# Performance work log

Hardware: AMD Instinct MI355X
Metric: run time of the kernel (lower is better)

The kernel has to match this reference:

```python
import jax, jax.numpy as jnp
import numpy as np

B, N, D = 16, 2048, 128  # batch, nodes, embedding_dim

def setup_inputs() -> dict:
    key = jax.random.key(0)
    ks = jax.random.split(key, 12)
    def dense(kw, kb, din, dout):
        # keras Dense default glorot_uniform weight, zeros bias (use small random bias for generality)
        lim = np.sqrt(6.0 / (din + dout))
        W = jax.random.uniform(kw, (din, dout), minval=-lim, maxval=lim, dtype=jnp.float32)
        b = jax.random.normal(kb, (dout,), dtype=jnp.float32) * 0.01
        return W, b
    Wq, bq = dense(ks[0], ks[1], D, D)
    Wk, bk = dense(ks[2], ks[3], D, D)
    Wv, bv = dense(ks[4], ks[5], D, D)
    Wo, bo = dense(ks[6], ks[7], D, D)
    query_ = jax.random.normal(ks[8], (B, N, D), dtype=jnp.float32)
    key_ = jax.random.normal(ks[9], (B, N, D), dtype=jnp.float32)
    mask = jax.random.randint(ks[10], (B, N + 1, N + 1), 0, 2).astype(bool)
    return {"query_": query_, "key_": key_, "mask": mask,
            "Wq": Wq, "bq": bq, "Wk": Wk, "bk": bk,
            "Wv": Wv, "bv": bv, "Wo": Wo, "bo": bo}

def reference(query_, key_, mask, Wq, bq, Wk, bk, Wv, bv, Wo, bo):
    q = query_ @ Wq + bq                       # [B,N,D]
    k = key_ @ Wk + bk                         # [B,N,D]
    comp = jnp.einsum('bqd,bkd->bqk', q, k)    # [B,N,N]
    comp = comp / jnp.sqrt(jnp.asarray(k.shape[-1], jnp.float32))
    m = mask[:, 1:, 1:]                        # [B,N,N]
    comp = jnp.where(m, -jnp.inf, comp)
    attn = jax.nn.softmax(comp, axis=-1)
    attn = jnp.where(jnp.isnan(attn), 0.0, attn)  # fully-masked rows -> 0
    # NOTE: faithful to source: value projection applied to the PROJECTED key
    v = k @ Wv + bv                            # [B,N,D]
    out = jnp.einsum('bqk,bkd->bqd', attn, v)
    return out @ Wo + bo
```

## Files before the change

### kernel.cpp

```cpp
#include <hip/hip_runtime.h>

#define SB 16
#define SN 2048
#define SD 128
#define NM 2049
#define SZ (SB*SN*SD)
#define WLDS 17408

typedef __bf16 bf16x8 __attribute__((ext_vector_type(8)));
typedef float f32x4 __attribute__((ext_vector_type(4)));

__device__ __forceinline__ unsigned short f2b(float f){
  union { float f; unsigned int u; } v; v.f = f;
  unsigned int r = v.u + 0x7fffu + ((v.u >> 16) & 1u);
  return (unsigned short)(r >> 16);
}
__device__ __forceinline__ unsigned short f2b_fast(float f){
  union { float f; unsigned int u; } v; v.f = f;
  return (unsigned short)((v.u + 0x8000u) >> 16);
}

__device__ __forceinline__ void async16(const void* g, void* l){
  __builtin_amdgcn_global_load_lds(
      (__attribute__((address_space(1))) void*)(g),
      (__attribute__((address_space(3))) void*)(l), 16, 0, 0);
}

__global__ __launch_bounds__(256) void prep_pack_kernel(
    const float* __restrict__ Wq, const float* __restrict__ Wk,
    const float* __restrict__ Wv, const float* __restrict__ Wo,
    const int* __restrict__ mask,
    unsigned short* __restrict__ wts, unsigned long long* __restrict__ pm)
{
  if (blockIdx.x < 64){
    int widx = blockIdx.x >> 4;
    int kg   = blockIdx.x & 15;
    const float* W = (widx==0)?Wq:(widx==1)?Wk:(widx==2)?Wv:Wo;
    unsigned short* O = wts + widx*16384;
    int t = threadIdx.x;
    int k = kg*8 + (t>>5);
    int n = (t&31)*4;
    float4 v = *reinterpret_cast<const float4*>(W + k*SD + n);
    O[(n+0)*SD + k] = f2b(v.x);
    O[(n+1)*SD + k] = f2b(v.y);
    O[(n+2)*SD + k] = f2b(v.z);
    O[(n+3)*SD + k] = f2b(v.w);
    return;
  }
  int widx = blockIdx.x - 64;
  int wave = widx*4 + (threadIdx.x>>6);
  int ln = threadIdx.x & 63;
  size_t wb0 = (size_t)wave*256;
  for (int rr=0; rr<32; rr++){
    size_t wb = wb0 + rr*8;
    int v[8];
    for (int i=0;i<8;i++){
      size_t wbi = wb + i;
      int bb = (int)(wbi>>16); int rem = (int)(wbi & 65535);
      int row = rem>>5; int kt = rem&31;
      v[i] = mask[(size_t)bb*NM*NM + (size_t)(row+1)*NM + 1 + kt*64 + ln];
    }
    unsigned long long bt[8];
    for (int i=0;i<8;i++) bt[i] = __ballot(v[i]!=0);
    if (ln==0){
      for (int i=0;i<4;i++){
        ulonglong2 t; t.x = bt[2*i]; t.y = bt[2*i+1];
        *reinterpret_cast<ulonglong2*>(&pm[wb + 2*i]) = t;
      }
    }
  }
}

__global__ __launch_bounds__(256) void qkv_kernel(
    const float* __restrict__ query, const float* __restrict__ key,
    const unsigned short* __restrict__ wts,
    const float* __restrict__ bq, const float* __restrict__ bk,
    const float* __restrict__ bv,
    unsigned short* __restrict__ qb, unsigned short* __restrict__ kb,
    unsigned short* __restrict__ vt)
{
  __shared__ unsigned short lds[2*WLDS + 9216];
  int tid=threadIdx.x;
  int w=tid>>6, ln=tid&63, g=ln>>4, lm=ln&15;
  bool isq = blockIdx.x < 512;
  int id = isq ? blockIdx.x : (blockIdx.x - 512);
  int bb = id>>5, n0 = (id&31)*64;
  size_t rowbase = (size_t)bb*SN + n0 + w*16;
  const float sc = 0.08838834764831845f;

  if (isq){
    for (int i=0;i<8;i++){
      int p = i*256+tid; int row=p>>4, c=p&15;
      uint4 t = *reinterpret_cast<const uint4*>(wts + p*8);
      *reinterpret_cast<uint4*>(&lds[row*136 + c*8]) = t;
    }
    __syncthreads();
    float bqv[8];
    for (int d=0;d<8;d++) bqv[d] = bq[d*16+lm];
    const float* xr = query + (rowbase + lm)*SD;
    bf16x8 af[4];
    for (int ks=0;ks<4;ks++){
      float4 x0 = *reinterpret_cast<const float4*>(xr + ks*32 + g*8);
      float4 x1 = *reinterpret_cast<const float4*>(xr + ks*32 + g*8 + 4);
      union { bf16x8 v; unsigned short s[8]; } u;
      u.s[0]=f2b(x0.x); u.s[1]=f2b(x0.y); u.s[2]=f2b(x0.z); u.s[3]=f2b(x0.w);
      u.s[4]=f2b(x1.x); u.s[5]=f2b(x1.y); u.s[6]=f2b(x1.z); u.s[7]=f2b(x1.w);
      af[ks]=u.v;
    }
    for (int d=0; d<8; d++){
      f32x4 acc = {0.f,0.f,0.f,0.f};
      for (int ks=0;ks<4;ks++){
        bf16x8 wf = *reinterpret_cast<const bf16x8*>(&lds[(d*16+lm)*136 + ks*32 + g*8]);
        acc = __builtin_amdgcn_mfma_f32_16x16x32_bf16(af[ks], wf, acc, 0,0,0);
      }
      for (int r=0;r<4;r++)
        qb[(rowbase + 4*g + r)*SD + d*16 + lm] = f2b((acc[r]+bqv[d])*sc);
    }
  } else {
    for (int i=0;i<8;i++){
      int p = i*256+tid; int row=p>>4, c=p&15;
      uint4 t = *reinterpret_cast<const uint4*>(wts + 16384 + p*8);
      *reinterpret_cast<uint4*>(&lds[row*136 + c*8]) = t;
    }
    for (int i=0;i<8;i++){
      int p = i*256+tid; int row=p>>4, c=p&15;
      uint4 t = *reinterpret_cast<const uint4*>(wts + 32768 + p*8);
      *reinterpret_cast<uint4*>(&lds[WLDS + row*136 + c*8]) = t;
    }
    __syncthreads();
    float bkv[8], bvv[8];
    for (int d=0;d<8;d++){ bkv[d]=bk[d*16+lm]; bvv[d]=bv[d*16+lm]; }
    const float* xr = key + (rowbase + lm)*SD;
    bf16x8 af[4];
    for (int ks=0;ks<4;ks++){
      float4 x0 = *reinterpret_cast<const float4*>(xr + ks*32 + g*8);
      float4 x1 = *reinterpret_cast<const float4*>(xr + ks*32 + g*8 + 4);
      union { bf16x8 v; unsigned short s[8]; } u;
      u.s[0]=f2b(x0.x); u.s[1]=f2b(x0.y); u.s[2]=f2b(x0.z); u.s[3]=f2b(x0.w);
      u.s[4]=f2b(x1.x); u.s[5]=f2b(x1.y); u.s[6]=f2b(x1.z); u.s[7]=f2b(x1.w);
      af[ks]=u.v;
    }
    unsigned short* strip = &lds[2*WLDS + w*2176];
    for (int d=0; d<8; d++){
      f32x4 acc = {0.f,0.f,0.f,0.f};
      for (int ks=0;ks<4;ks++){
        bf16x8 wf = *reinterpret_cast<const bf16x8*>(&lds[(d*16+lm)*136 + ks*32 + g*8]);
        acc = __builtin_amdgcn_mfma_f32_16x16x32_bf16(af[ks], wf, acc, 0,0,0);
      }
      for (int r=0;r<4;r++){
        unsigned short kv2 = f2b(acc[r]+bkv[d]);
        kb[(rowbase + 4*g + r)*SD + d*16 + lm] = kv2;
        strip[(4*g+r)*136 + d*16 + lm] = kv2;
      }
    }
    bf16x8 ka[4];
    for (int ks=0;ks<4;ks++)
      ka[ks] = *reinterpret_cast<const bf16x8*>(&strip[lm*136 + ks*32 + g*8]);
    __syncthreads();
    unsigned short* vT = &lds[2*WLDS];
    for (int d=0; d<8; d++){
      f32x4 acc = {0.f,0.f,0.f,0.f};
      for (int ks=0;ks<4;ks++){
        bf16x8 wf = *reinterpret_cast<const bf16x8*>(&lds[WLDS + (d*16+lm)*136 + ks*32 + g*8]);
        acc = __builtin_amdgcn_mfma_f32_16x16x32_bf16(ka[ks], wf, acc, 0,0,0);
      }
      ushort4 pk;
      pk.x=f2b(acc[0]+bvv[d]); pk.y=f2b(acc[1]+bvv[d]);
      pk.z=f2b(acc[2]+bvv[d]); pk.w=f2b(acc[3]+bvv[d]);
      *reinterpret_cast<ushort4*>(&vT[(d*16+lm)*72 + w*16 + 4*g]) = pk;
    }
    __syncthreads();
    for (int i=0;i<4;i++){
      int idx = i*256+tid; int row = idx>>3, c8 = idx&7;
      uint4 t = *reinterpret_cast<const uint4*>(&vT[row*72 + c8*8]);
      *reinterpret_cast<uint4*>(vt + (size_t)bb*SD*SN + (size_t)row*SN + n0 + c8*8) = t;
    }
  }
}

__global__ __launch_bounds__(256,4) void flash_kernel(
    const unsigned short* __restrict__ qb, const unsigned short* __restrict__ kb,
    const unsigned short* __restrict__ vt, const unsigned long long* __restrict__ pm,
    const unsigned short* __restrict__ WoT, const float* __restrict__ bo,
    float* __restrict__ out)
{
  __shared__ unsigned short bufK[2][64*128];
  __shared__ unsigned short bufV[2][128*64];
  __shared__ unsigned short ldsP[4*16*72];

  int tid=threadIdx.x;
  int w=tid>>6, ln=tid&63, g=ln>>4, lm=ln&15;
  int b = blockIdx.x >> 5, qt = blockIdx.x & 31;
  int q0 = qt*64;

  const unsigned short* Qb = qb + (size_t)b*SN*SD;
  const unsigned short* Kb = kb + (size_t)b*SN*SD;
  const unsigned short* Vb = vt + (size_t)b*SD*SN;

  auto issueK = [&](int k0, int bi){
    const char* gbase = (const char*)Kb + (size_t)k0*256;
    for (int c=0;c<4;c++){
      int p = c*256 + tid;
      int row = p>>4, lc = (p&15) ^ (row&15);
      async16(gbase + (size_t)row*256 + lc*16, (char*)bufK[bi] + p*16);
    }
  };
  auto issueV = [&](int k0, int bi){
    const char* gbase = (const char*)Vb + (size_t)k0*2;
    for (int c=0;c<4;c++){
      int p = c*256 + tid;
      int row = p>>3, lc = (p&7) ^ (row&7);
      async16(gbase + (size_t)row*4096 + lc*16, (char*)bufV[bi] + p*16);
    }
  };

  issueK(0,0); issueV(0,0);

  bf16x8 qf[4];
  {
    const unsigned short* qr = Qb + (size_t)(q0 + w*16 + lm)*SD;
    for (int ks=0;ks<4;ks++)
      qf[ks] = *reinterpret_cast<const bf16x8*>(qr + ks*32 + g*8);
  }

  const unsigned long long* pmr = pm + ((size_t)b*SN + q0 + w*16 + 4*g)*32;
  unsigned long long pmc[4];
  for (int r=0;r<4;r++) pmc[r] = pmr[(size_t)r*32];

  float mrow[4], lrow[4], al[4];
  f32x4 acc[8];
  for (int r=0;r<4;r++){ mrow[r]=-INFINITY; lrow[r]=0.f; }
  for (int d=0;d<8;d++){ f32x4 z={0.f,0.f,0.f,0.f}; acc[d]=z; }
  unsigned short* pw = &ldsP[w*16*72];

  for (int kt=0; kt<32; kt++){
    __syncthreads();
    int cur = kt&1;
    if (kt<31){ issueK((kt+1)*64, cur^1); issueV((kt+1)*64, cur^1); }

    f32x4 s[4];
    for (int ct=0;ct<4;ct++){
      f32x4 z = {0.f,0.f,0.f,0.f};
      for (int ks=0;ks<4;ks++){
        bf16x8 kf = *reinterpret_cast<const bf16x8*>(
            &bufK[cur][(ct*16+lm)*128 + (((ks*4+g)^lm))*8]);
        z = __builtin_amdgcn_mfma_f32_16x16x32_bf16(qf[ks], kf, z, 0,0,0);
      }
      s[ct]=z;
    }

    for (int r=0;r<4;r++){
      unsigned int lo = (unsigned int)pmc[r];
      unsigned int hi = (unsigned int)(pmc[r]>>32);
      unsigned int l = lo >> lm, h = hi >> lm;
      if (l & 1u)       s[0][r] = -INFINITY;
      if (l & 0x10000u) s[1][r] = -INFINITY;
      if (h & 1u)       s[2][r] = -INFINITY;
      if (h & 0x10000u) s[3][r] = -INFINITY;
    }
    if (kt<31)
      for (int r=0;r<4;r++) pmc[r] = pmr[(size_t)r*32 + kt + 1];

    for (int r=0;r<4;r++){
      float v = fmaxf(fmaxf(s[0][r],s[1][r]), fmaxf(s[2][r],s[3][r]));
      v = fmaxf(v, __shfl_xor(v,1,16));
      v = fmaxf(v, __shfl_xor(v,2,16));
      v = fmaxf(v, __shfl_xor(v,4,16));
      v = fmaxf(v, __shfl_xor(v,8,16));
      float mn = fmaxf(mrow[r], v);
      bool dead = (mn == -INFINITY);
      float a = dead ? 1.f : __expf(mrow[r]-mn);
      float rsum = 0.f;
      for (int ct=0;ct<4;ct++){
        float p = dead ? 0.f : __expf(s[ct][r]-mn);
        s[ct][r]=p; rsum += p;
      }
      rsum += __shfl_xor(rsum,1,16);
      rsum += __shfl_xor(rsum,2,16);
      rsum += __shfl_xor(rsum,4,16);
      rsum += __shfl_xor(rsum,8,16);
      lrow[r] = lrow[r]*a + rsum;
      mrow[r] = mn;
      al[r] = a;
    }
    for (int d=0;d<8;d++)
      for (int r=0;r<4;r++)
        acc[d][r] *= al[r];

    for (int ct=0;ct<4;ct++){
      int col = ct*16+lm;
      for (int r=0;r<4;r++)
        pw[(4*g+r)*72 + col] = f2b_fast(s[ct][r]);
    }
    bf16x8 pa0 = *reinterpret_cast<const bf16x8*>(&pw[lm*72 + g*8]);
    bf16x8 pa1 = *reinterpret_cast<const bf16x8*>(&pw[lm*72 + 32 + g*8]);

    for (int d=0;d<8;d++){
      bf16x8 v0 = *reinterpret_cast<const bf16x8*>(
          &bufV[cur][(d*16+lm)*64 + ((g^(lm&7)))*8]);
      acc[d] = __builtin_amdgcn_mfma_f32_16x16x32_bf16(pa0, v0, acc[d], 0,0,0);
      bf16x8 v1 = *reinterpret_cast<const bf16x8*>(
          &bufV[cur][(d*16+lm)*64 + (((4+g)^(lm&7)))*8]);
      acc[d] = __builtin_amdgcn_mfma_f32_16x16x32_bf16(pa1, v1, acc[d], 0,0,0);
    }
  }

  __syncthreads();
  float inv[4];
  for (int r=0;r<4;r++) inv[r] = (lrow[r] > 0.f) ? (1.f/lrow[r]) : 0.f;
  unsigned short* strip = &bufK[0][0] + w*2176;
  for (int d=0;d<8;d++)
    for (int r=0;r<4;r++)
      strip[(4*g+r)*136 + d*16 + lm] = f2b(acc[d][r]*inv[r]);
  bf16x8 oa[4];
  for (int ks=0;ks<4;ks++)
    oa[ks] = *reinterpret_cast<const bf16x8*>(&strip[lm*136 + ks*32 + g*8]);
  float* Ob = out + ((size_t)b*SN + q0 + w*16)*SD;
  for (int dc=0; dc<8; dc++){
    f32x4 o = {0.f,0.f,0.f,0.f};
    for (int ks=0;ks<4;ks++){
      bf16x8 wf = *reinterpret_cast<const bf16x8*>(WoT + (dc*16+lm)*SD + ks*32 + g*8);
      o = __builtin_amdgcn_mfma_f32_16x16x32_bf16(oa[ks], wf, o, 0,0,0);
    }
    float bb = bo[dc*16+lm];
    for (int r=0;r<4;r++)
      Ob[(size_t)(4*g+r)*SD + dc*16 + lm] = o[r]+bb;
  }
}

extern "C" void kernel_launch(void* const* d_in, const int* in_sizes, int n_in,
                              void* d_out, int out_size, void* d_ws, size_t ws_size,
                              hipStream_t stream)
{
  const float* query = (const float*)d_in[0];
  const float* key   = (const float*)d_in[1];
  const int*   mask  = (const int*)d_in[2];
  const float* Wq = (const float*)d_in[3];
  const float* bq = (const float*)d_in[4];
  const float* Wk = (const float*)d_in[5];
  const float* bk = (const float*)d_in[6];
  const float* Wv = (const float*)d_in[7];
  const float* bv = (const float*)d_in[8];
  const float* Wo = (const float*)d_in[9];
  const float* bo = (const float*)d_in[10];
  float* out = (float*)d_out;

  unsigned short* qb = (unsigned short*)d_ws;
  unsigned short* kb = qb + SZ;
  unsigned short* vt = kb + SZ;
  unsigned short* wts = vt + SZ;
  unsigned long long* pm = (unsigned long long*)(wts + 65536);

  prep_pack_kernel<<<1088,256,0,stream>>>(Wq,Wk,Wv,Wo, mask, wts, pm);
  qkv_kernel      <<<1024,256,0,stream>>>(query, key, wts, bq, bk, bv, qb, kb, vt);
  flash_kernel    <<<512,256,0,stream>>>(qb, kb, vt, pm, wts+49152, bo, out);
}
```

Baseline: 519.7 us.

## Split QKV projection into 16-row blocks with per-wave weight slices in registers

The QKV projection kernel now launches 4096 blocks, each handling 16 rows instead of 64. Each wave owns two 16-column output groups and loads its weight fragments straight from global memory into registers, replacing the block-wide LDS staging of full weight matrices. This shrinks LDS use and raises parallelism and occupancy. In exchange, the weights are re-read from global or cache by many more blocks, and the transposed V store writes only 32 bytes per column row per block.

After: 542.0 us. 1.04x slower.

```diff
diff --git a/kernel.cpp b/kernel.cpp
--- a/kernel.cpp
+++ b/kernel.cpp
@@ -5,7 +5,6 @@
 #define SD 128
 #define NM 2049
 #define SZ (SB*SN*SD)
-#define WLDS 17408
 
 typedef __bf16 bf16x8 __attribute__((ext_vector_type(8)));
 typedef float f32x4 __attribute__((ext_vector_type(4)));
@@ -79,24 +78,25 @@
     unsigned short* __restrict__ qb, unsigned short* __restrict__ kb,
     unsigned short* __restrict__ vt)
 {
-  __shared__ unsigned short lds[2*WLDS + 9216];
+  __shared__ unsigned short kstrip[16*136];
+  __shared__ unsigned short vstrip[128*24];
+
   int tid=threadIdx.x;
   int w=tid>>6, ln=tid&63, g=ln>>4, lm=ln&15;
-  bool isq = blockIdx.x < 512;
-  int id = isq ? blockIdx.x : (blockIdx.x - 512);
-  int bb = id>>5, n0 = (id&31)*64;
-  size_t rowbase = (size_t)bb*SN + n0 + w*16;
+  bool isq = blockIdx.x < 2048;
+  int id = isq ? blockIdx.x : (blockIdx.x - 2048);
+  int bb = id>>7, n0 = (id&127)*16;
+  size_t rowbase = (size_t)bb*SN + n0;
   const float sc = 0.08838834764831845f;
 
   if (isq){
-    for (int i=0;i<8;i++){
-      int p = i*256+tid; int row=p>>4, c=p&15;
-      uint4 t = *reinterpret_cast<const uint4*>(wts + p*8);
-      *reinterpret_cast<uint4*>(&lds[row*136 + c*8]) = t;
-    }
-    __syncthreads();
-    float bqv[8];
-    for (int d=0;d<8;d++) bqv[d] = bq[d*16+lm];
+    bf16x8 wq[2][4];
+    for (int dg=0;dg<2;dg++){
+      int d = w*2+dg;
+      for (int ks=0;ks<4;ks++)
+        wq[dg][ks] = *reinterpret_cast<const bf16x8*>(wts + (d*16+lm)*SD + ks*32 + g*8);
+    }
+    float bqv[2] = { bq[(w*2)*16+lm], bq[(w*2+1)*16+lm] };
     const float* xr = query + (rowbase + lm)*SD;
     bf16x8 af[4];
     for (int ks=0;ks<4;ks++){
@@ -107,29 +107,25 @@
       u.s[4]=f2b(x1.x); u.s[5]=f2b(x1.y); u.s[6]=f2b(x1.z); u.s[7]=f2b(x1.w);
       af[ks]=u.v;
     }
-    for (int d=0; d<8; d++){
+    for (int dg=0;dg<2;dg++){
+      int d = w*2+dg;
       f32x4 acc = {0.f,0.f,0.f,0.f};
+      for (int ks=0;ks<4;ks++)
+        acc = __builtin_amdgcn_mfma_f32_16x16x32_bf16(af[ks], wq[dg][ks], acc, 0,0,0);
+      for (int r=0;r<4;r++)
+        qb[(rowbase + 4*g + r)*SD + d*16 + lm] = f2b((acc[r]+bqv[dg])*sc);
+    }
+  } else {
+    bf16x8 wk[2][4], wv[2][4];
+    for (int dg=0;dg<2;dg++){
+      int d = w*2+dg;
       for (int ks=0;ks<4;ks++){
-        bf16x8 wf = *reinterpret_cast<const bf16x8*>(&lds[(d*16+lm)*136 + ks*32 + g*8]);
-        acc = __builtin_amdgcn_mfma_f32_16x16x32_bf16(af[ks], wf, acc, 0,0,0);
-      }
-      for (int r=0;r<4;r++)
-        qb[(rowbase + 4*g + r)*SD + d*16 + lm] = f2b((acc[r]+bqv[d])*sc);
-    }
-  } else {
-    for (int i=0;i<8;i++){
-      int p = i*256+tid; int row=p>>4, c=p&15;
-      uint4 t = *reinterpret_cast<const uint4*>(wts + 16384 + p*8);
-      *reinterpret_cast<uint4*>(&lds[row*136 + c*8]) = t;
-    }
-    for (int i=0;i<8;i++){
-      int p = i*256+tid; int row=p>>4, c=p&15;
-      uint4 t = *reinterpret_cast<const uint4*>(wts + 32768 + p*8);
-      *reinterpret_cast<uint4*>(&lds[WLDS + row*136 + c*8]) = t;
-    }
-    __syncthreads();
-    float bkv[8], bvv[8];
-    for (int d=0;d<8;d++){ bkv[d]=bk[d*16+lm]; bvv[d]=bv[d*16+lm]; }
+        wk[dg][ks] = *reinterpret_cast<const bf16x8*>(wts + 16384 + (d*16+lm)*SD + ks*32 + g*8);
+        wv[dg][ks] = *reinterpret_cast<const bf16x8*>(wts + 32768 + (d*16+lm)*SD + ks*32 + g*8);
+      }
+    }
+    float bkv[2] = { bk[(w*2)*16+lm], bk[(w*2+1)*16+lm] };
+    float bvv[2] = { bv[(w*2)*16+lm], bv[(w*2+1)*16+lm] };
     const float* xr = key + (rowbase + lm)*SD;
     bf16x8 af[4];
     for (int ks=0;ks<4;ks++){
@@ -140,41 +136,35 @@
       u.s[4]=f2b(x1.x); u.s[5]=f2b(x1.y); u.s[6]=f2b(x1.z); u.s[7]=f2b(x1.w);
       af[ks]=u.v;
     }
-    unsigned short* strip = &lds[2*WLDS + w*2176];
-    for (int d=0; d<8; d++){
+    for (int dg=0;dg<2;dg++){
+      int d = w*2+dg;
       f32x4 acc = {0.f,0.f,0.f,0.f};
-      for (int ks=0;ks<4;ks++){
-        bf16x8 wf = *reinterpret_cast<const bf16x8*>(&lds[(d*16+lm)*136 + ks*32 + g*8]);
-        acc = __builtin_amdgcn_mfma_f32_16x16x32_bf16(af[ks], wf, acc, 0,0,0);
-      }
+      for (int ks=0;ks<4;ks++)
+        acc = __builtin_amdgcn_mfma_f32_16x16x32_bf16(af[ks], wk[dg][ks], acc, 0,0,0);
       for (int r=0;r<4;r++){
-        unsigned short kv2 = f2b(acc[r]+bkv[d]);
+        unsigned short kv2 = f2b(acc[r]+bkv[dg]);
         kb[(rowbase + 4*g + r)*SD + d*16 + lm] = kv2;
-        strip[(4*g+r)*136 + d*16 + lm] = kv2;
-      }
-    }
+        kstrip[(4*g+r)*136 + d*16 + lm] = kv2;
+      }
+    }
+    __syncthreads();
     bf16x8 ka[4];
     for (int ks=0;ks<4;ks++)
-      ka[ks] = *reinterpret_cast<const bf16x8*>(&strip[lm*136 + ks*32 + g*8]);
+      ka[ks] = *reinterpret_cast<const bf16x8*>(&kstrip[lm*136 + ks*32 + g*8]);
+    for (int dg=0;dg<2;dg++){
+      int d = w*2+dg;
+      f32x4 acc = {0.f,0.f,0.f,0.f};
+      for (int ks=0;ks<4;ks++)
+        acc = __builtin_amdgcn_mfma_f32_16x16x32_bf16(ka[ks], wv[dg][ks], acc, 0,0,0);
+      ushort4 pk;
+      pk.x=f2b(acc[0]+bvv[dg]); pk.y=f2b(acc[1]+bvv[dg]);
+      pk.z=f2b(acc[2]+bvv[dg]); pk.w=f2b(acc[3]+bvv[dg]);
+      *reinterpret_cast<ushort4*>(&vstrip[(d*16+lm)*24 + 4*g]) = pk;
+    }
     __syncthreads();
-    unsigned short* vT = &lds[2*WLDS];
-    for (int d=0; d<8; d++){
-      f32x4 acc = {0.f,0.f,0.f,0.f};
-      for (int ks=0;ks<4;ks++){
-        bf16x8 wf = *reinterpret_cast<const bf16x8*>(&lds[WLDS + (d*16+lm)*136 + ks*32 + g*8]);
-        acc = __builtin_amdgcn_mfma_f32_16x16x32_bf16(ka[ks], wf, acc, 0,0,0);
-      }
-      ushort4 pk;
-      pk.x=f2b(acc[0]+bvv[d]); pk.y=f2b(acc[1]+bvv[d]);
-      pk.z=f2b(acc[2]+bvv[d]); pk.w=f2b(acc[3]+bvv[d]);
-      *reinterpret_cast<ushort4*>(&vT[(d*16+lm)*72 + w*16 + 4*g]) = pk;
-    }
-    __syncthreads();
-    for (int i=0;i<4;i++){
-      int idx = i*256+tid; int row = idx>>3, c8 = idx&7;
-      uint4 t = *reinterpret_cast<const uint4*>(&vT[row*72 + c8*8]);
-      *reinterpret_cast<uint4*>(vt + (size_t)bb*SD*SN + (size_t)row*SN + n0 + c8*8) = t;
-    }
+    int col = tid>>1, half = tid&1;
+    uint4 t = *reinterpret_cast<const uint4*>(&vstrip[col*24 + half*8]);
+    *reinterpret_cast<uint4*>(vt + (size_t)bb*SD*SN + (size_t)col*SN + n0 + half*8) = t;
   }
 }
 
@@ -352,6 +342,6 @@
   unsigned long long* pm = (unsigned long long*)(wts + 65536);
 
   prep_pack_kernel<<<1088,256,0,stream>>>(Wq,Wk,Wv,Wo, mask, wts, pm);
-  qkv_kernel      <<<1024,256,0,stream>>>(query, key, wts, bq, bk, bv, qb, kb, vt);
+  qkv_kernel      <<<4096,256,0,stream>>>(query, key, wts, bq, bk, bv, qb, kb, vt);
   flash_kernel    <<<512,256,0,stream>>>(qb, kb, vt, pm, wts+49152, bo, out);
 }
```
